# Kernel tuning notes

Hardware: AMD Instinct MI355X
Metric: run time of the kernel (lower is better)

## Reference

```python
import jax, jax.numpy as jnp
import numpy as np

N = 262144
EMBED = 64            # embed_size
EDGE_H = 256          # edge_hidden_size
NODE_H = 128          # node_hidden_size
LSTM_IN = 2 * EMBED   # concat(e_v, a_v)


def setup_inputs() -> dict:
    key = jax.random.key(0)
    ks = jax.random.split(key, 14)
    s = 0.05
    return {
        "Hv_t": jax.random.normal(ks[0], (N, EDGE_H), jnp.float32),
        "hvv_t": jax.random.normal(ks[1], (N, EDGE_H), jnp.float32),
        "xv_t": jax.random.normal(ks[2], (N, 2), jnp.float32),
        "hv_tm1": jax.random.normal(ks[3], (N, NODE_H), jnp.float32),
        "cv_tm1": jax.random.normal(ks[4], (N, NODE_H), jnp.float32),
        "ts_mask": jax.random.randint(ks[5], (N, 1), 0, 2, jnp.int32),
        # pos_embed: Linear(2 -> EMBED)
        "W_pos": jax.random.normal(ks[6], (EMBED, 2), jnp.float32) * s,
        "b_pos": jax.random.normal(ks[7], (EMBED,), jnp.float32) * s,
        # hid_embed: Linear(2*EDGE_H -> EMBED)
        "W_hid": jax.random.normal(ks[8], (EMBED, 2 * EDGE_H), jnp.float32) * s,
        "b_hid": jax.random.normal(ks[9], (EMBED,), jnp.float32) * s,
        # LSTM(LSTM_IN -> NODE_H), PyTorch layout: gates order i,f,g,o
        "W_ih": jax.random.normal(ks[10], (4 * NODE_H, LSTM_IN), jnp.float32) * s,
        "b_ih": jax.random.normal(ks[11], (4 * NODE_H,), jnp.float32) * s,
        "W_hh": jax.random.normal(ks[12], (4 * NODE_H, NODE_H), jnp.float32) * s,
        "b_hh": jax.random.normal(ks[13], (4 * NODE_H,), jnp.float32) * s,
    }


def reference(Hv_t, hvv_t, xv_t, hv_tm1, cv_tm1, ts_mask,
              W_pos, b_pos, W_hid, b_hid, W_ih, b_ih, W_hh, b_hh):
    # Active-node mask (N, 1). Torch gathers active rows, runs one LSTM step,
    # and scatters back; equivalently compute everywhere and select with the mask.
    mask = (ts_mask[:, 0] == 1)[:, None]

    e_v = jax.nn.relu(xv_t @ W_pos.T + b_pos)                              # (N, EMBED)
    a_v = jax.nn.relu(jnp.concatenate([hvv_t, Hv_t], axis=1) @ W_hid.T + b_hid)  # (N, EMBED)
    x = jnp.concatenate([e_v, a_v], axis=1)                                # (N, 2*EMBED)

    # Single-step LSTM cell (PyTorch gate order: i, f, g, o)
    gates = x @ W_ih.T + b_ih + hv_tm1 @ W_hh.T + b_hh                     # (N, 4*NODE_H)
    i, f, g, o = jnp.split(gates, 4, axis=1)
    i = jax.nn.sigmoid(i)
    f = jax.nn.sigmoid(f)
    g = jnp.tanh(g)
    o = jax.nn.sigmoid(o)
    c_new = f * cv_tm1 + i * g
    h_new = o * jnp.tanh(c_new)

    hv_t = jnp.where(mask, h_new, hv_tm1)
    cv_t = jnp.where(mask, c_new, cv_tm1)
    return hv_t, cv_t
```

## Files before the change

kernel.cpp:

```cpp
#include <hip/hip_runtime.h>

#define N_NODES 262144
#define BM 64
#define NTHREADS 512

typedef short s16x8 __attribute__((ext_vector_type(8)));
typedef float f32x4 __attribute__((ext_vector_type(4)));

static __device__ __forceinline__ unsigned short f2bf(float f) {
  union { float f; unsigned u; } v; v.f = f;
  unsigned u = v.u;
  u += 0x7FFFu + ((u >> 16) & 1u);
  return (unsigned short)(u >> 16);
}

static __device__ __forceinline__ unsigned long long pack4bf(f32x4 v) {
  unsigned u0 = (unsigned)f2bf(v.x) | ((unsigned)f2bf(v.y) << 16);
  unsigned u1 = (unsigned)f2bf(v.z) | ((unsigned)f2bf(v.w) << 16);
  return (unsigned long long)u0 | ((unsigned long long)u1 << 32);
}

static __device__ __forceinline__ float fsig(float x) {
  return __builtin_amdgcn_rcpf(1.0f + __expf(-x));
}
static __device__ __forceinline__ float ftanh(float x) {
  return 2.0f * __builtin_amdgcn_rcpf(1.0f + __expf(-2.0f * x)) - 1.0f;
}

__global__ void prep_kernel(const float* __restrict__ Whid, const float* __restrict__ Wih,
                            const float* __restrict__ Whh, const float* __restrict__ bih,
                            const float* __restrict__ bhh,
                            unsigned short* __restrict__ oWh2, unsigned short* __restrict__ oW2,
                            float* __restrict__ oBias) {
  int t = blockIdx.x * 256 + threadIdx.x;
  if (t < 32768) {
    int kb = t >> 11, n = (t >> 5) & 63, ki = t & 31;
    oWh2[t] = f2bf(Whid[n * 512 + kb * 32 + ki]);
  }
  if (t < 131072) {
    int kb = t >> 14, n = (t >> 5) & 511, ki = t & 31;
    int k = kb * 32 + ki;
    float v = (k < 128) ? Wih[n * 128 + k] : Whh[n * 128 + (k - 128)];
    oW2[t] = f2bf(v);
  }
  if (t < 512) oBias[t] = bih[t] + bhh[t];
}

#define SWZA(m, b) ((((m) * 1024) + (b)) ^ (((m) & 7) << 4))
#define SWZ2(m, b) ((((m) * 512) + (b)) ^ (((m) & 7) << 4))

__global__ __launch_bounds__(NTHREADS, 4) void node_rnn_kernel(
    const float* __restrict__ Hv, const float* __restrict__ hvv,
    const float* __restrict__ xv, const float* __restrict__ hvp,
    const float* __restrict__ cvp, const int* __restrict__ tsm,
    const float* __restrict__ Wpos, const float* __restrict__ bpos,
    const float* __restrict__ bhid,
    const unsigned short* __restrict__ Wh2,
    const unsigned short* __restrict__ W2,
    const float* __restrict__ biasg,
    float* __restrict__ hvo, float* __restrict__ cvo)
{
  __shared__ __align__(16) char lds[65536];

  const int tid = threadIdx.x;
  const int w   = tid >> 6;
  const int l   = tid & 63;
  const int l15 = l & 15;
  const int lk  = l >> 4;
  const int wr  = w >> 2;
  const int wc  = w & 3;
  const int node0 = blockIdx.x * BM;

#pragma unroll
  for (int it = 0; it < 16; ++it) {
    int p = tid + it * NTHREADS;
    int m = p >> 7, ch = p & 127;
    const float* src = (ch < 64) ? (hvv + (size_t)(node0 + m) * 256 + ch * 4)
                                 : (Hv  + (size_t)(node0 + m) * 256 + (ch - 64) * 4);
    f32x4 v = *(const f32x4*)src;
    *(unsigned long long*)(lds + SWZA(m, ch * 8)) = pack4bf(v);
  }

  float ev[8];
#pragma unroll
  for (int it = 0; it < 8; ++it) {
    int p = tid + it * NTHREADS;
    int m = p >> 6, j = p & 63;
    float x0 = xv[(size_t)(node0 + m) * 2 + 0];
    float x1 = xv[(size_t)(node0 + m) * 2 + 1];
    ev[it] = fmaxf(x0 * Wpos[j * 2 + 0] + x1 * Wpos[j * 2 + 1] + bpos[j], 0.0f);
  }
  f32x4 hvc[4];
#pragma unroll
  for (int it = 0; it < 4; ++it) {
    int p = tid + it * NTHREADS;
    int m = p >> 5, c4 = p & 31;
    hvc[it] = *(const f32x4*)(hvp + (size_t)(node0 + m) * 128 + c4 * 4);
  }

  __syncthreads();

  f32x4 acc[2] = {f32x4{0.f,0.f,0.f,0.f}, f32x4{0.f,0.f,0.f,0.f}};
  {
    const char* whb = (const char*)Wh2 + (wc * 16 + l15) * 64 + lk * 16;
#pragma unroll
    for (int ks = 0; ks < 16; ++ks) {
      s16x8 bf = *(const s16x8*)(whb + ks * 4096);
#pragma unroll
      for (int mi = 0; mi < 2; ++mi) {
        int m = wr * 32 + mi * 16 + l15;
        s16x8 af = *(const s16x8*)(lds + SWZA(m, ks * 64 + lk * 16));
        acc[mi] = __builtin_amdgcn_mfma_f32_16x16x32_bf16(af, bf, acc[mi], 0, 0, 0);
      }
    }
  }

  __syncthreads();

#pragma unroll
  for (int it = 0; it < 8; ++it) {
    int p = tid + it * NTHREADS;
    int m = p >> 6, j = p & 63;
    *(unsigned short*)(lds + SWZ2(m, j * 2)) = f2bf(ev[it]);
  }
#pragma unroll
  for (int it = 0; it < 4; ++it) {
    int p = tid + it * NTHREADS;
    int m = p >> 5, c4 = p & 31;
    *(unsigned long long*)(lds + SWZ2(m, 256 + c4 * 8)) = pack4bf(hvc[it]);
  }
  {
    float bb = bhid[wc * 16 + l15];
    int cb = (64 + wc * 16 + l15) * 2;
#pragma unroll
    for (int mi = 0; mi < 2; ++mi) {
#pragma unroll
      for (int r = 0; r < 4; ++r) {
        int m = wr * 32 + mi * 16 + lk * 4 + r;
        float av = fmaxf(acc[mi][r] + bb, 0.0f);
        *(unsigned short*)(lds + SWZ2(m, cb)) = f2bf(av);
      }
    }
  }
  __syncthreads();

  f32x4 acc2[4][4];
#pragma unroll
  for (int mi = 0; mi < 4; ++mi)
#pragma unroll
    for (int j = 0; j < 4; ++j) acc2[mi][j] = f32x4{0.f,0.f,0.f,0.f};

#pragma unroll
  for (int kk = 0; kk < 8; ++kk) {
    s16x8 a[4];
#pragma unroll
    for (int mi = 0; mi < 4; ++mi)
      a[mi] = *(const s16x8*)(lds + SWZ2(mi * 16 + l15, kk * 64 + lk * 16));
    const char* wb = (const char*)W2 + kk * 32768 + lk * 16;
#pragma unroll
    for (int j = 0; j < 4; ++j) {
      s16x8 bf = *(const s16x8*)(wb + (size_t)(16 * w + 128 * j + l15) * 64);
#pragma unroll
      for (int mi = 0; mi < 4; ++mi)
        acc2[mi][j] = __builtin_amdgcn_mfma_f32_16x16x32_bf16(a[mi], bf, acc2[mi][j], 0, 0, 0);
    }
  }

  float bs[4];
#pragma unroll
  for (int j = 0; j < 4; ++j) bs[j] = biasg[128 * j + 16 * w + l15];
  const int d = 16 * w + l15;

#pragma unroll
  for (int mi = 0; mi < 4; ++mi) {
#pragma unroll
    for (int r = 0; r < 4; ++r) {
      int m = mi * 16 + lk * 4 + r;
      size_t node = (size_t)node0 + m;
      int act = tsm[node];
      float gi = acc2[mi][0][r] + bs[0];
      float gf = acc2[mi][1][r] + bs[1];
      float gg = acc2[mi][2][r] + bs[2];
      float go = acc2[mi][3][r] + bs[3];
      float i_ = fsig(gi), f_ = fsig(gf), o_ = fsig(go);
      float g_ = ftanh(gg);
      float co = cvp[node * 128 + d];
      float ho = hvp[node * 128 + d];
      float cn = f_ * co + i_ * g_;
      float hn = o_ * ftanh(cn);
      hvo[node * 128 + d] = act ? hn : ho;
      cvo[node * 128 + d] = act ? cn : co;
    }
  }
}

extern "C" void kernel_launch(void* const* d_in, const int* in_sizes, int n_in,
                              void* d_out, int out_size, void* d_ws, size_t ws_size,
                              hipStream_t stream) {
  const float* Hv   = (const float*)d_in[0];
  const float* hvv  = (const float*)d_in[1];
  const float* xv   = (const float*)d_in[2];
  const float* hvp  = (const float*)d_in[3];
  const float* cvp  = (const float*)d_in[4];
  const int*   tsm  = (const int*)d_in[5];
  const float* Wpos = (const float*)d_in[6];
  const float* bpos = (const float*)d_in[7];
  const float* Whid = (const float*)d_in[8];
  const float* bhid = (const float*)d_in[9];
  const float* Wih  = (const float*)d_in[10];
  const float* bih  = (const float*)d_in[11];
  const float* Whh  = (const float*)d_in[12];
  const float* bhh  = (const float*)d_in[13];

  unsigned short* wsWh2 = (unsigned short*)d_ws;
  unsigned short* wsW2  = wsWh2 + 32768;
  float* wsBias = (float*)(wsW2 + 131072);

  prep_kernel<<<512, 256, 0, stream>>>(Whid, Wih, Whh, bih, bhh,
                                       wsWh2, wsW2, wsBias);

  float* hvo = (float*)d_out;
  float* cvo = hvo + (size_t)N_NODES * 128;
  node_rnn_kernel<<<N_NODES / BM, NTHREADS, 0, stream>>>(
      Hv, hvv, xv, hvp, cvp, tsm, Wpos, bpos, bhid,
      wsWh2, wsW2, wsBias, hvo, cvo);
}
```

Measured before the change: 284.6 us.

## Halve block tile and double-buffer the hidden-embed K loop in LDS

Measured after the change: 403.7 us. 41.9% more time.

```diff
diff --git a/kernel.cpp b/kernel.cpp
--- a/kernel.cpp
+++ b/kernel.cpp
@@ -1,8 +1,8 @@
 #include <hip/hip_runtime.h>
 
 #define N_NODES 262144
-#define BM 64
-#define NTHREADS 512
+#define BM 32
+#define NTHREADS 256
 
 typedef short s16x8 __attribute__((ext_vector_type(8)));
 typedef float f32x4 __attribute__((ext_vector_type(4)));
@@ -46,8 +46,7 @@
   if (t < 512) oBias[t] = bih[t] + bhh[t];
 }
 
-#define SWZA(m, b) ((((m) * 1024) + (b)) ^ (((m) & 7) << 4))
-#define SWZ2(m, b) ((((m) * 512) + (b)) ^ (((m) & 7) << 4))
+#define SWZ(m, b) ((((m) * 512) + (b)) ^ (((m) & 7) << 4))
 
 __global__ __launch_bounds__(NTHREADS, 4) void node_rnn_kernel(
     const float* __restrict__ Hv, const float* __restrict__ hvv,
@@ -60,25 +59,31 @@
     const float* __restrict__ biasg,
     float* __restrict__ hvo, float* __restrict__ cvo)
 {
-  __shared__ __align__(16) char lds[65536];
+  __shared__ __align__(16) char lds[32768];
+  char* buf0 = lds;
+  char* buf1 = lds + 16384;
 
   const int tid = threadIdx.x;
   const int w   = tid >> 6;
   const int l   = tid & 63;
   const int l15 = l & 15;
   const int lk  = l >> 4;
-  const int wr  = w >> 2;
-  const int wc  = w & 3;
   const int node0 = blockIdx.x * BM;
 
 #pragma unroll
-  for (int it = 0; it < 16; ++it) {
-    int p = tid + it * NTHREADS;
-    int m = p >> 7, ch = p & 127;
-    const float* src = (ch < 64) ? (hvv + (size_t)(node0 + m) * 256 + ch * 4)
-                                 : (Hv  + (size_t)(node0 + m) * 256 + (ch - 64) * 4);
-    f32x4 v = *(const f32x4*)src;
-    *(unsigned long long*)(lds + SWZA(m, ch * 8)) = pack4bf(v);
+  for (int it = 0; it < 8; ++it) {
+    int p = tid + it * NTHREADS;
+    int m = p >> 6, ch = p & 63;
+    f32x4 v = *(const f32x4*)(hvv + (size_t)(node0 + m) * 256 + ch * 4);
+    *(unsigned long long*)(buf0 + SWZ(m, ch * 8)) = pack4bf(v);
+  }
+
+  f32x4 gv[8];
+#pragma unroll
+  for (int it = 0; it < 8; ++it) {
+    int p = tid + it * NTHREADS;
+    int m = p >> 6, ch = p & 63;
+    gv[it] = *(const f32x4*)(Hv + (size_t)(node0 + m) * 256 + ch * 4);
   }
 
   float ev[8];
@@ -101,95 +106,119 @@
   __syncthreads();
 
   f32x4 acc[2] = {f32x4{0.f,0.f,0.f,0.f}, f32x4{0.f,0.f,0.f,0.f}};
+  const char* whb = (const char*)Wh2 + (16 * w + l15) * 64 + lk * 16;
+#pragma unroll
+  for (int ks = 0; ks < 8; ++ks) {
+    s16x8 bf = *(const s16x8*)(whb + ks * 4096);
+#pragma unroll
+    for (int mi = 0; mi < 2; ++mi) {
+      s16x8 af = *(const s16x8*)(buf0 + SWZ(mi * 16 + l15, ks * 64 + lk * 16));
+      acc[mi] = __builtin_amdgcn_mfma_f32_16x16x32_bf16(af, bf, acc[mi], 0, 0, 0);
+    }
+  }
+
+#pragma unroll
+  for (int it = 0; it < 8; ++it) {
+    int p = tid + it * NTHREADS;
+    int m = p >> 6, ch = p & 63;
+    *(unsigned long long*)(buf1 + SWZ(m, ch * 8)) = pack4bf(gv[it]);
+  }
+
+  __syncthreads();
+
+#pragma unroll
+  for (int ks = 0; ks < 8; ++ks) {
+    s16x8 bf = *(const s16x8*)(whb + (8 + ks) * 4096);
+#pragma unroll
+    for (int mi = 0; mi < 2; ++mi) {
+      s16x8 af = *(const s16x8*)(buf1 + SWZ(mi * 16 + l15, ks * 64 + lk * 16));
+      acc[mi] = __builtin_amdgcn_mfma_f32_16x16x32_bf16(af, bf, acc[mi], 0, 0, 0);
+    }
+  }
+
+#pragma unroll
+  for (int it = 0; it < 8; ++it) {
+    int p = tid + it * NTHREADS;
+    int m = p >> 6, j = p & 63;
+    *(unsigned short*)(buf0 + SWZ(m, j * 2)) = f2bf(ev[it]);
+  }
+#pragma unroll
+  for (int it = 0; it < 4; ++it) {
+    int p = tid + it * NTHREADS;
+    int m = p >> 5, c4 = p & 31;
+    *(unsigned long long*)(buf0 + SWZ(m, 256 + c4 * 8)) = pack4bf(hvc[it]);
+  }
   {
-    const char* whb = (const char*)Wh2 + (wc * 16 + l15) * 64 + lk * 16;
-#pragma unroll
-    for (int ks = 0; ks < 16; ++ks) {
-      s16x8 bf = *(const s16x8*)(whb + ks * 4096);
-#pragma unroll
-      for (int mi = 0; mi < 2; ++mi) {
-        int m = wr * 32 + mi * 16 + l15;
-        s16x8 af = *(const s16x8*)(lds + SWZA(m, ks * 64 + lk * 16));
-        acc[mi] = __builtin_amdgcn_mfma_f32_16x16x32_bf16(af, bf, acc[mi], 0, 0, 0);
+    float bb = bhid[16 * w + l15];
+    int cb = (64 + 16 * w + l15) * 2;
+#pragma unroll
+    for (int mi = 0; mi < 2; ++mi) {
+#pragma unroll
+      for (int r = 0; r < 4; ++r) {
+        int m = mi * 16 + lk * 4 + r;
+        float av = fmaxf(acc[mi][r] + bb, 0.0f);
+        *(unsigned short*)(buf0 + SWZ(m, cb)) = f2bf(av);
       }
     }
   }
-
   __syncthreads();
 
-#pragma unroll
-  for (int it = 0; it < 8; ++it) {
-    int p = tid + it * NTHREADS;
-    int m = p >> 6, j = p & 63;
-    *(unsigned short*)(lds + SWZ2(m, j * 2)) = f2bf(ev[it]);
-  }
-#pragma unroll
-  for (int it = 0; it < 4; ++it) {
-    int p = tid + it * NTHREADS;
-    int m = p >> 5, c4 = p & 31;
-    *(unsigned long long*)(lds + SWZ2(m, 256 + c4 * 8)) = pack4bf(hvc[it]);
-  }
-  {
-    float bb = bhid[wc * 16 + l15];
-    int cb = (64 + wc * 16 + l15) * 2;
-#pragma unroll
-    for (int mi = 0; mi < 2; ++mi) {
-#pragma unroll
-      for (int r = 0; r < 4; ++r) {
-        int m = wr * 32 + mi * 16 + lk * 4 + r;
-        float av = fmaxf(acc[mi][r] + bb, 0.0f);
-        *(unsigned short*)(lds + SWZ2(m, cb)) = f2bf(av);
+  f32x4 acc2[2][4][2];
+#pragma unroll
+  for (int mi = 0; mi < 2; ++mi)
+#pragma unroll
+    for (int j = 0; j < 4; ++j)
+#pragma unroll
+      for (int h = 0; h < 2; ++h) acc2[mi][j][h] = f32x4{0.f,0.f,0.f,0.f};
+
+#pragma unroll
+  for (int kk = 0; kk < 8; ++kk) {
+    s16x8 a[2];
+#pragma unroll
+    for (int mi = 0; mi < 2; ++mi)
+      a[mi] = *(const s16x8*)(buf0 + SWZ(mi * 16 + l15, kk * 64 + lk * 16));
+    const char* wb = (const char*)W2 + kk * 32768 + (16 * w + l15) * 64 + lk * 16;
+#pragma unroll
+    for (int j = 0; j < 4; ++j) {
+#pragma unroll
+      for (int h = 0; h < 2; ++h) {
+        s16x8 bf = *(const s16x8*)(wb + (size_t)(128 * j + 64 * h) * 64);
+#pragma unroll
+        for (int mi = 0; mi < 2; ++mi)
+          acc2[mi][j][h] = __builtin_amdgcn_mfma_f32_16x16x32_bf16(a[mi], bf, acc2[mi][j][h], 0, 0, 0);
       }
     }
   }
-  __syncthreads();
-
-  f32x4 acc2[4][4];
-#pragma unroll
-  for (int mi = 0; mi < 4; ++mi)
-#pragma unroll
-    for (int j = 0; j < 4; ++j) acc2[mi][j] = f32x4{0.f,0.f,0.f,0.f};
-
-#pragma unroll
-  for (int kk = 0; kk < 8; ++kk) {
-    s16x8 a[4];
-#pragma unroll
-    for (int mi = 0; mi < 4; ++mi)
-      a[mi] = *(const s16x8*)(lds + SWZ2(mi * 16 + l15, kk * 64 + lk * 16));
-    const char* wb = (const char*)W2 + kk * 32768 + lk * 16;
-#pragma unroll
-    for (int j = 0; j < 4; ++j) {
-      s16x8 bf = *(const s16x8*)(wb + (size_t)(16 * w + 128 * j + l15) * 64);
-#pragma unroll
-      for (int mi = 0; mi < 4; ++mi)
-        acc2[mi][j] = __builtin_amdgcn_mfma_f32_16x16x32_bf16(a[mi], bf, acc2[mi][j], 0, 0, 0);
-    }
-  }
-
-  float bs[4];
-#pragma unroll
-  for (int j = 0; j < 4; ++j) bs[j] = biasg[128 * j + 16 * w + l15];
-  const int d = 16 * w + l15;
-
-#pragma unroll
-  for (int mi = 0; mi < 4; ++mi) {
+
+  float bs[4][2];
+#pragma unroll
+  for (int j = 0; j < 4; ++j)
+#pragma unroll
+    for (int h = 0; h < 2; ++h) bs[j][h] = biasg[128 * j + 64 * h + 16 * w + l15];
+
+#pragma unroll
+  for (int mi = 0; mi < 2; ++mi) {
 #pragma unroll
     for (int r = 0; r < 4; ++r) {
       int m = mi * 16 + lk * 4 + r;
       size_t node = (size_t)node0 + m;
       int act = tsm[node];
-      float gi = acc2[mi][0][r] + bs[0];
-      float gf = acc2[mi][1][r] + bs[1];
-      float gg = acc2[mi][2][r] + bs[2];
-      float go = acc2[mi][3][r] + bs[3];
-      float i_ = fsig(gi), f_ = fsig(gf), o_ = fsig(go);
-      float g_ = ftanh(gg);
-      float co = cvp[node * 128 + d];
-      float ho = hvp[node * 128 + d];
-      float cn = f_ * co + i_ * g_;
-      float hn = o_ * ftanh(cn);
-      hvo[node * 128 + d] = act ? hn : ho;
-      cvo[node * 128 + d] = act ? cn : co;
+#pragma unroll
+      for (int h = 0; h < 2; ++h) {
+        int d = 16 * w + 64 * h + l15;
+        float gi = acc2[mi][0][h][r] + bs[0][h];
+        float gf = acc2[mi][1][h][r] + bs[1][h];
+        float gg = acc2[mi][2][h][r] + bs[2][h];
+        float go = acc2[mi][3][h][r] + bs[3][h];
+        float i_ = fsig(gi), f_ = fsig(gf), o_ = fsig(go);
+        float g_ = ftanh(gg);
+        float co = cvp[node * 128 + d];
+        float ho = hvp[node * 128 + d];
+        float cn = f_ * co + i_ * g_;
+        float hn = o_ * ftanh(cn);
+        hvo[node * 128 + d] = act ? hn : ho;
+        cvo[node * 128 + d] = act ? cn : co;
+      }
     }
   }
 }
```

## Split LSTM GEMM into two halves, prefetch state, ballot mask, hardware bf16 pack

Applied to the files above, without the earlier changes.

After: 448.5 us. 1.58x slower.

```diff
diff --git a/kernel.cpp b/kernel.cpp
--- a/kernel.cpp
+++ b/kernel.cpp
@@ -6,6 +6,12 @@
 
 typedef short s16x8 __attribute__((ext_vector_type(8)));
 typedef float f32x4 __attribute__((ext_vector_type(4)));
+
+static __device__ __forceinline__ unsigned cvtpk(float lo, float hi) {
+  unsigned r;
+  asm("v_cvt_pk_bf16_f32 %0, %1, %2" : "=v"(r) : "v"(lo), "v"(hi));
+  return r;
+}
 
 static __device__ __forceinline__ unsigned short f2bf(float f) {
   union { float f; unsigned u; } v; v.f = f;
@@ -15,8 +21,8 @@
 }
 
 static __device__ __forceinline__ unsigned long long pack4bf(f32x4 v) {
-  unsigned u0 = (unsigned)f2bf(v.x) | ((unsigned)f2bf(v.y) << 16);
-  unsigned u1 = (unsigned)f2bf(v.z) | ((unsigned)f2bf(v.w) << 16);
+  unsigned u0 = cvtpk(v.x, v.y);
+  unsigned u1 = cvtpk(v.z, v.w);
   return (unsigned long long)u0 | ((unsigned long long)u1 << 32);
 }
 
@@ -70,6 +76,7 @@
   const int wr  = w >> 2;
   const int wc  = w & 3;
   const int node0 = blockIdx.x * BM;
+  const int d   = 16 * w + l15;
 
 #pragma unroll
   for (int it = 0; it < 16; ++it) {
@@ -81,14 +88,18 @@
     *(unsigned long long*)(lds + SWZA(m, ch * 8)) = pack4bf(v);
   }
 
-  float ev[8];
-#pragma unroll
-  for (int it = 0; it < 8; ++it) {
-    int p = tid + it * NTHREADS;
-    int m = p >> 6, j = p & 63;
+  unsigned long long actmask = __ballot(tsm[node0 + l] == 1);
+
+  unsigned evp[4];
+#pragma unroll
+  for (int it = 0; it < 4; ++it) {
+    int p = tid + it * NTHREADS;
+    int m = p >> 5, jp = p & 31;
     float x0 = xv[(size_t)(node0 + m) * 2 + 0];
     float x1 = xv[(size_t)(node0 + m) * 2 + 1];
-    ev[it] = fmaxf(x0 * Wpos[j * 2 + 0] + x1 * Wpos[j * 2 + 1] + bpos[j], 0.0f);
+    float e0 = fmaxf(x0 * Wpos[(2*jp  )*2] + x1 * Wpos[(2*jp  )*2+1] + bpos[2*jp  ], 0.f);
+    float e1 = fmaxf(x0 * Wpos[(2*jp+1)*2] + x1 * Wpos[(2*jp+1)*2+1] + bpos[2*jp+1], 0.f);
+    evp[it] = cvtpk(e0, e1);
   }
   f32x4 hvc[4];
 #pragma unroll
@@ -118,10 +129,10 @@
   __syncthreads();
 
 #pragma unroll
-  for (int it = 0; it < 8; ++it) {
-    int p = tid + it * NTHREADS;
-    int m = p >> 6, j = p & 63;
-    *(unsigned short*)(lds + SWZ2(m, j * 2)) = f2bf(ev[it]);
+  for (int it = 0; it < 4; ++it) {
+    int p = tid + it * NTHREADS;
+    int m = p >> 5, jp = p & 31;
+    *(unsigned*)(lds + SWZ2(m, jp * 4)) = evp[it];
   }
 #pragma unroll
   for (int it = 0; it < 4; ++it) {
@@ -144,52 +155,63 @@
   }
   __syncthreads();
 
-  f32x4 acc2[4][4];
+  float bs[4];
+#pragma unroll
+  for (int j = 0; j < 4; ++j) bs[j] = biasg[128 * j + d];
+  float cvv[4][4], hov[4][4];
 #pragma unroll
   for (int mi = 0; mi < 4; ++mi)
 #pragma unroll
-    for (int j = 0; j < 4; ++j) acc2[mi][j] = f32x4{0.f,0.f,0.f,0.f};
-
-#pragma unroll
-  for (int kk = 0; kk < 8; ++kk) {
-    s16x8 a[4];
-#pragma unroll
-    for (int mi = 0; mi < 4; ++mi)
-      a[mi] = *(const s16x8*)(lds + SWZ2(mi * 16 + l15, kk * 64 + lk * 16));
-    const char* wb = (const char*)W2 + kk * 32768 + lk * 16;
-#pragma unroll
-    for (int j = 0; j < 4; ++j) {
-      s16x8 bf = *(const s16x8*)(wb + (size_t)(16 * w + 128 * j + l15) * 64);
-#pragma unroll
-      for (int mi = 0; mi < 4; ++mi)
-        acc2[mi][j] = __builtin_amdgcn_mfma_f32_16x16x32_bf16(a[mi], bf, acc2[mi][j], 0, 0, 0);
-    }
-  }
-
-  float bs[4];
-#pragma unroll
-  for (int j = 0; j < 4; ++j) bs[j] = biasg[128 * j + 16 * w + l15];
-  const int d = 16 * w + l15;
-
-#pragma unroll
-  for (int mi = 0; mi < 4; ++mi) {
-#pragma unroll
     for (int r = 0; r < 4; ++r) {
-      int m = mi * 16 + lk * 4 + r;
-      size_t node = (size_t)node0 + m;
-      int act = tsm[node];
-      float gi = acc2[mi][0][r] + bs[0];
-      float gf = acc2[mi][1][r] + bs[1];
-      float gg = acc2[mi][2][r] + bs[2];
-      float go = acc2[mi][3][r] + bs[3];
-      float i_ = fsig(gi), f_ = fsig(gf), o_ = fsig(go);
-      float g_ = ftanh(gg);
-      float co = cvp[node * 128 + d];
-      float ho = hvp[node * 128 + d];
-      float cn = f_ * co + i_ * g_;
-      float hn = o_ * ftanh(cn);
-      hvo[node * 128 + d] = act ? hn : ho;
-      cvo[node * 128 + d] = act ? cn : co;
+      size_t node = (size_t)node0 + mi * 16 + lk * 4 + r;
+      cvv[mi][r] = cvp[node * 128 + d];
+      hov[mi][r] = hvp[node * 128 + d];
+    }
+
+#pragma unroll
+  for (int P = 0; P < 2; ++P) {
+    f32x4 acc2[2][4];
+#pragma unroll
+    for (int mi = 0; mi < 2; ++mi)
+#pragma unroll
+      for (int j = 0; j < 4; ++j) acc2[mi][j] = f32x4{0.f,0.f,0.f,0.f};
+
+#pragma unroll
+    for (int kk = 0; kk < 8; ++kk) {
+      s16x8 a[2];
+#pragma unroll
+      for (int mi = 0; mi < 2; ++mi)
+        a[mi] = *(const s16x8*)(lds + SWZ2((P * 2 + mi) * 16 + l15, kk * 64 + lk * 16));
+      const char* wb = (const char*)W2 + kk * 32768 + lk * 16;
+#pragma unroll
+      for (int j = 0; j < 4; ++j) {
+        s16x8 bf = *(const s16x8*)(wb + (size_t)(16 * w + 128 * j + l15) * 64);
+#pragma unroll
+        for (int mi = 0; mi < 2; ++mi)
+          acc2[mi][j] = __builtin_amdgcn_mfma_f32_16x16x32_bf16(a[mi], bf, acc2[mi][j], 0, 0, 0);
+      }
+    }
+
+#pragma unroll
+    for (int mi = 0; mi < 2; ++mi) {
+#pragma unroll
+      for (int r = 0; r < 4; ++r) {
+        int m = (P * 2 + mi) * 16 + lk * 4 + r;
+        size_t node = (size_t)node0 + m;
+        int act = (int)((actmask >> m) & 1ull);
+        float gi = acc2[mi][0][r] + bs[0];
+        float gf = acc2[mi][1][r] + bs[1];
+        float gg = acc2[mi][2][r] + bs[2];
+        float go = acc2[mi][3][r] + bs[3];
+        float i_ = fsig(gi), f_ = fsig(gf), o_ = fsig(go);
+        float g_ = ftanh(gg);
+        float co = cvv[P * 2 + mi][r];
+        float ho = hov[P * 2 + mi][r];
+        float cn = f_ * co + i_ * g_;
+        float hn = o_ * ftanh(cn);
+        hvo[node * 128 + d] = act ? hn : ho;
+        cvo[node * 128 + d] = act ? cn : co;
+      }
     }
   }
 }
```
